# Kernel tuning notes

Measured on AMD Instinct MI355X. Metric: run time of the kernel, lower is better.

## Reference

```python
import jax, jax.numpy as jnp
import numpy as np

N = 50000      # nodes per graph
E = 600000     # edges per graph
IN_DIM = 512
HID = 128
LAYERS = 2


def setup_inputs() -> dict:
    key = jax.random.key(0)
    ks = jax.random.split(key, 24)
    s = 0.05
    inp = {
        "src_fea": jax.random.normal(ks[0], (N, IN_DIM), jnp.float32),
        "trg_fea": jax.random.normal(ks[1], (N, IN_DIM), jnp.float32),
        "src_row": jax.random.randint(ks[2], (E,), 0, N, jnp.int32),
        "src_col": jax.random.randint(ks[3], (E,), 0, N, jnp.int32),
        "trg_row": jax.random.randint(ks[4], (E,), 0, N, jnp.int32),
        "trg_col": jax.random.randint(ks[5], (E,), 0, N, jnp.int32),
        # fx: Linear(in,hid)+GELU+Linear(hid,hid)+GELU
        "fxW1": jax.random.normal(ks[6], (IN_DIM, HID), jnp.float32) * s,
        "fxb1": jnp.zeros((HID,), jnp.float32),
        "fxW2": jax.random.normal(ks[7], (HID, HID), jnp.float32) * s,
        "fxb2": jnp.zeros((HID,), jnp.float32),
        # edge_att_mlp: Linear(2h,20)+ReLU+Linear(20,10)+ReLU+Linear(10,1)+ReLU
        "eaW1": jax.random.normal(ks[8], (2 * HID, 20), jnp.float32) * s,
        "eab1": jnp.zeros((20,), jnp.float32),
        "eaW2": jax.random.normal(ks[9], (20, 10), jnp.float32) * s,
        "eab2": jnp.zeros((10,), jnp.float32),
        "eaW3": jax.random.normal(ks[10], (10, 1), jnp.float32) * s,
        "eab3": jnp.zeros((1,), jnp.float32),
        # GraphConv (PyG-style, bias=False): out = x@Wroot + agg@Wrel
        "convWroot": jax.random.normal(ks[11], (LAYERS, HID, HID), jnp.float32) * s,
        "convWrel": jax.random.normal(ks[12], (LAYERS, HID, HID), jnp.float32) * s,
    }
    return inp


def _fx(x, W1, b1, W2, b2):
    h = jax.nn.gelu(x @ W1 + b1, approximate=False)
    return jax.nn.gelu(h @ W2 + b2, approximate=False)


def _edge_att(e, eaW1, eab1, eaW2, eab2, eaW3, eab3):
    h = jax.nn.relu(e @ eaW1 + eab1)
    h = jax.nn.relu(h @ eaW2 + eab2)
    h = jax.nn.relu(h @ eaW3 + eab3)
    return jax.nn.sigmoid(h)  # [E,1]


def _graph_conv(x, row, col, ew, Wroot, Wrel):
    # message from source (row) gathered, weighted, aggregated at target (col)
    msg = ew[:, None] * x[row]                                  # [E,h]
    agg = jax.ops.segment_sum(msg, col, num_segments=N)         # [N,h]
    return x @ Wroot + agg @ Wrel


def _branch(x0, row, col, convWroot, convWrel, eaW1, eab1, eaW2, eab2, eaW3, eab3, hard):
    xs, cfds = [], []
    x = x0
    for i in range(LAYERS):
        edge_rep = jnp.concatenate([x[row], x[col]], axis=-1)    # [E,2h]
        att = _edge_att(edge_rep, eaW1, eab1, eaW2, eab2, eaW3, eab3)[:, 0]
        wc = (att + hard) * 0.5
        wo = 1.0 - wc
        x = jax.nn.soft_sign(_graph_conv(x, row, col, wc, convWroot[i], convWrel[i]))
        cfd = jax.nn.soft_sign(_graph_conv(x, row, col, wo, convWroot[i], convWrel[i]))
        xs.append(x)
        cfds.append(cfd)
    return xs, cfds


def reference(src_fea, trg_fea, src_row, src_col, trg_row, trg_col,
              fxW1, fxb1, fxW2, fxb2,
              eaW1, eab1, eaW2, eab2, eaW3, eab3,
              convWroot, convWrel):
    src1 = _fx(src_fea, fxW1, fxb1, fxW2, fxb2)
    trg1 = _fx(trg_fea, fxW1, fxb1, fxW2, fxb2)
    ea = (eaW1, eab1, eaW2, eab2, eaW3, eab3)
    xs_s, cf_s = _branch(src1, src_row, src_col, convWroot, convWrel, *ea, 0.0)
    xs_t, cf_t = _branch(trg1, trg_row, trg_col, convWroot, convWrel, *ea, 0.0)
    # stack: [src1, xs_s..., trg1, xs_t..., cf_s..., cf_t...] -> [2+2*LAYERS+2*LAYERS? no: 10, N, h]
    return jnp.stack([src1] + xs_s + [trg1] + xs_t + cf_s + cf_t, axis=0)
```

## Files before the change

### kernel.cpp

```cpp
#include <hip/hip_runtime.h>
#include <math.h>
#include <stdint.h>


typedef __attribute__((ext_vector_type(8))) short bh8;
typedef __attribute__((ext_vector_type(4))) float f4;

__device__ __forceinline__ float relu_f(float x) { return x > 0.f ? x : 0.f; }

__device__ __forceinline__ unsigned short f2bf(float f) {
    union { float f; unsigned u; } v; v.f = f;
    unsigned r = v.u + 0x7FFF + ((v.u >> 16) & 1);
    return (unsigned short)(r >> 16);
}
__device__ __forceinline__ float bf2f(unsigned short b) {
    union { unsigned u; float f; } v; v.u = ((unsigned)b) << 16;
    return v.f;
}

template<int ACT>
__device__ __forceinline__ float act_fn(float x) {
    if (ACT == 1) return 0.5f * x * (1.f + erff(x * 0.70710678118654752f));
    if (ACT == 2) return x / (1.f + fabsf(x));
    return x;
}

template<int K, int AF, int ACT, bool DUAL, bool BIAS, bool WF32, bool WB16>
__global__ __launch_bounds__(256, 2)
void mfma_gemm(const void* __restrict__ X0a, const void* __restrict__ X1a,
               const void* __restrict__ X0b, const void* __restrict__ X1b,
               const short* __restrict__ W0t, const short* __restrict__ W1t,
               const float* __restrict__ bias,
               float* __restrict__ outfA, short* __restrict__ outbA,
               float* __restrict__ outfB, short* __restrict__ outbB, int M)
{
    constexpr int BK  = 64;
    constexpr int LDA = 72;
    __shared__ short As[64 * LDA];
    __shared__ short Bs[128 * LDA];

    const int half = gridDim.x >> 1;
    int bid = blockIdx.x;
    const int g1 = bid >= half;
    bid -= g1 ? half : 0;
    const void* X0v = g1 ? X0b : X0a;
    const void* X1v = g1 ? X1b : X1a;
    float* outf = g1 ? outfB : outfA;
    short* outb = g1 ? outbB : outbA;

    const int t    = threadIdx.x;
    const int row0 = bid * 64;
    const int lane = t & 63;
    const int w    = t >> 6;
    const int wr   = w & 1;
    const int wc   = w >> 1;
    const int l15  = lane & 15;
    const int l4   = lane >> 4;

    f4 acc[2][4];
    #pragma unroll
    for (int i = 0; i < 2; ++i)
        #pragma unroll
        for (int j = 0; j < 4; ++j)
            acc[i][j] = (f4){0.f, 0.f, 0.f, 0.f};

    const int ar = t >> 3;
    const int ac = (t & 7) * 8;

    #pragma unroll 1
    for (int s = 0; s < (DUAL ? 2 : 1); ++s) {
        const float* Xf = (const float*)((DUAL && s) ? X1v : X0v);
        const short* Xb = (const short*)((DUAL && s) ? X1v : X0v);
        const short* Wt = (DUAL && s) ? W1t : W0t;
        #pragma unroll 1
        for (int k0 = 0; k0 < K; k0 += BK) {
            __syncthreads();
            #pragma unroll
            for (int p = 0; p < 2; ++p) {
                int r    = ar + p * 32;
                int grow = row0 + r;
                bh8 sv = {0, 0, 0, 0, 0, 0, 0, 0};
                if (AF == 0) {
                    if (grow < M) {
                        const float* src = Xf + (size_t)grow * K + k0 + ac;
                        float4 v0 = *(const float4*)src;
                        float4 v1 = *(const float4*)(src + 4);
                        sv[0] = (short)f2bf(v0.x); sv[1] = (short)f2bf(v0.y);
                        sv[2] = (short)f2bf(v0.z); sv[3] = (short)f2bf(v0.w);
                        sv[4] = (short)f2bf(v1.x); sv[5] = (short)f2bf(v1.y);
                        sv[6] = (short)f2bf(v1.z); sv[7] = (short)f2bf(v1.w);
                    }
                } else {
                    if (grow < M)
                        sv = *(const bh8*)(Xb + (size_t)grow * K + k0 + ac);
                }
                *(bh8*)&As[r * LDA + ac] = sv;
            }
            #pragma unroll
            for (int p = 0; p < 4; ++p) {
                int r = ar + p * 32;
                *(bh8*)&Bs[r * LDA + ac] =
                    *(const bh8*)(Wt + (size_t)r * K + k0 + ac);
            }
            __syncthreads();
            #pragma unroll
            for (int kk = 0; kk < 2; ++kk) {
                bh8 a[2], b[4];
                #pragma unroll
                for (int mi = 0; mi < 2; ++mi)
                    a[mi] = *(const bh8*)&As[(wr*32 + mi*16 + l15) * LDA + kk*32 + l4*8];
                #pragma unroll
                for (int ni = 0; ni < 4; ++ni)
                    b[ni] = *(const bh8*)&Bs[(wc*64 + ni*16 + l15) * LDA + kk*32 + l4*8];
                #pragma unroll
                for (int mi = 0; mi < 2; ++mi)
                    #pragma unroll
                    for (int ni = 0; ni < 4; ++ni)
                        acc[mi][ni] = __builtin_amdgcn_mfma_f32_16x16x32_bf16(
                            a[mi], b[ni], acc[mi][ni], 0, 0, 0);
            }
        }
    }

    #pragma unroll
    for (int mi = 0; mi < 2; ++mi) {
        #pragma unroll
        for (int ni = 0; ni < 4; ++ni) {
            int col = wc * 64 + ni * 16 + l15;
            float bv = BIAS ? bias[col] : 0.f;
            #pragma unroll
            for (int r = 0; r < 4; ++r) {
                int row = row0 + wr * 32 + mi * 16 + l4 * 4 + r;
                if (row < M) {
                    float v = act_fn<ACT>(acc[mi][ni][r] + bv);
                    if (WF32) outf[(size_t)row * 128 + col] = v;
                    if (WB16) outb[(size_t)row * 128 + col] = (short)f2bf(v);
                }
            }
        }
    }
}

__global__ __launch_bounds__(256, 2)
void pkern_both(const short* __restrict__ XbS, const short* __restrict__ XbT,
                const short* __restrict__ W56,
                short* __restrict__ PS, short* __restrict__ PT, int M)
{
    constexpr int LDA = 72;
    __shared__ short As[64 * LDA];
    __shared__ short Bs[64 * LDA];

    const int half = gridDim.x >> 1;
    int bid = blockIdx.x;
    const int g1 = bid >= half;
    bid -= g1 ? half : 0;
    const short* Xb = g1 ? XbT : XbS;
    short* P        = g1 ? PT  : PS;

    const int t    = threadIdx.x;
    const int row0 = bid * 64;
    const int lane = t & 63;
    const int w    = t >> 6;
    const int l15  = lane & 15;
    const int l4   = lane >> 4;

    f4 acc[4];
    #pragma unroll
    for (int i = 0; i < 4; ++i) acc[i] = (f4){0.f, 0.f, 0.f, 0.f};

    const int ar = t >> 3;
    const int ac = (t & 7) * 8;

    #pragma unroll 1
    for (int k0 = 0; k0 < 128; k0 += 64) {
        __syncthreads();
        #pragma unroll
        for (int p = 0; p < 2; ++p) {
            int r    = ar + p * 32;
            int grow = row0 + r;
            bh8 sv = {0, 0, 0, 0, 0, 0, 0, 0};
            if (grow < M)
                sv = *(const bh8*)(Xb + (size_t)grow * 128 + k0 + ac);
            *(bh8*)&As[r * LDA + ac] = sv;
        }
        #pragma unroll
        for (int p = 0; p < 2; ++p) {
            int r = ar + p * 32;
            *(bh8*)&Bs[r * LDA + ac] =
                *(const bh8*)(W56 + (size_t)r * 128 + k0 + ac);
        }
        __syncthreads();
        #pragma unroll
        for (int kk = 0; kk < 2; ++kk) {
            bh8 a = *(const bh8*)&As[(w * 16 + l15) * LDA + kk * 32 + l4 * 8];
            #pragma unroll
            for (int ni = 0; ni < 4; ++ni) {
                bh8 b = *(const bh8*)&Bs[(ni * 16 + l15) * LDA + kk * 32 + l4 * 8];
                acc[ni] = __builtin_amdgcn_mfma_f32_16x16x32_bf16(a, b, acc[ni], 0, 0, 0);
            }
        }
    }

    #pragma unroll
    for (int ni = 0; ni < 4; ++ni) {
        int col = ni * 16 + l15;
        #pragma unroll
        for (int r = 0; r < 4; ++r) {
            int row = row0 + w * 16 + l4 * 4 + r;
            if (row < M)
                P[(size_t)row * 64 + col] = (short)f2bf(acc[ni][r]);
        }
    }
}

__global__ void prep_all(const float* __restrict__ eaW1, const float* __restrict__ fxW1,
                         const float* __restrict__ fxW2, const float* __restrict__ convWroot,
                         const float* __restrict__ convWrel,
                         short* __restrict__ w56, short* __restrict__ fxW1t,
                         short* __restrict__ fxW2t, short* __restrict__ wrt,
                         short* __restrict__ wlt)
{
    int i = blockIdx.x * 256 + threadIdx.x;
    if (i < 64 * 128) {
        int j = i >> 7, k = i & 127;
        float v = 0.f;
        if (j < 20)                  v = eaW1[k * 20 + j];
        else if (j >= 32 && j < 52)  v = eaW1[(128 + k) * 20 + (j - 32)];
        w56[i] = (short)f2bf(v);
        return;
    }
    i -= 64 * 128;
    if (i < 512 * 128) {
        int k = i >> 7, n = i & 127;
        fxW1t[(size_t)n * 512 + k] = (short)f2bf(fxW1[i]);
        return;
    }
    i -= 512 * 128;
    if (i < 128 * 128) {
        int k = i >> 7, n = i & 127;
        fxW2t[n * 128 + k] = (short)f2bf(fxW2[i]);
        return;
    }
    i -= 128 * 128;
    if (i < 2 * 128 * 128) {
        int L = i >> 14, r = i & 16383;
        int k = r >> 7, n = r & 127;
        wrt[L * 16384 + n * 128 + k] = (short)f2bf(convWroot[i]);
        return;
    }
    i -= 2 * 128 * 128;
    if (i < 2 * 128 * 128) {
        int L = i >> 14, r = i & 16383;
        int k = r >> 7, n = r & 127;
        wlt[L * 16384 + n * 128 + k] = (short)f2bf(convWrel[i]);
    }
}

__global__ __launch_bounds__(256)
void edge_att_both(const short* __restrict__ PS, const short* __restrict__ PT,
                   const int* __restrict__ rowS, const int* __restrict__ colS,
                   const int* __restrict__ rowT, const int* __restrict__ colT,
                   const int* __restrict__ eposS, const int* __restrict__ eposT,
                   const float* __restrict__ eab1, const float* __restrict__ eaW2,
                   const float* __restrict__ eab2, const float* __restrict__ eaW3,
                   const float* __restrict__ eab3,
                   float* __restrict__ attcS, float* __restrict__ attcT, int E)
{
    __shared__ float w2[200], b2s[10], w3s[10], sb1[20], sb3;
    int t = threadIdx.x;
    if (t < 200) w2[t] = eaW2[t];
    if (t < 20)  sb1[t] = eab1[t];
    if (t < 10)  { b2s[t] = eab2[t]; w3s[t] = eaW3[t]; }
    if (t == 0)  sb3 = eab3[0];
    __syncthreads();

    int idx = blockIdx.x * 256 + t;
    if (idx >= 2 * E) return;
    const int g1 = idx >= E;
    const int e  = idx - (g1 ? E : 0);
    const short* P    = g1 ? PT : PS;
    const int*   row  = g1 ? rowT : rowS;
    const int*   col  = g1 ? colT : colS;
    const int*   epos = g1 ? eposT : eposS;
    float*       attc = g1 ? attcT : attcS;

    int r = row[e], c = col[e];
    const unsigned short* p1 = (const unsigned short*)P + (size_t)r * 64;
    const unsigned short* p2 = (const unsigned short*)P + (size_t)c * 64 + 32;

    bh8 a0 = *(const bh8*)&p1[0];
    bh8 a1 = *(const bh8*)&p1[8];
    ushort4 a2 = *(const ushort4*)&p1[16];
    bh8 b0 = *(const bh8*)&p2[0];
    bh8 b1 = *(const bh8*)&p2[8];
    ushort4 b2 = *(const ushort4*)&p2[16];

    float h1[20];
    #pragma unroll
    for (int j = 0; j < 8; ++j)
        h1[j] = relu_f(bf2f((unsigned short)a0[j]) + bf2f((unsigned short)b0[j]) + sb1[j]);
    #pragma unroll
    for (int j = 0; j < 8; ++j)
        h1[8 + j] = relu_f(bf2f((unsigned short)a1[j]) + bf2f((unsigned short)b1[j]) + sb1[8 + j]);
    h1[16] = relu_f(bf2f(a2.x) + bf2f(b2.x) + sb1[16]);
    h1[17] = relu_f(bf2f(a2.y) + bf2f(b2.y) + sb1[17]);
    h1[18] = relu_f(bf2f(a2.z) + bf2f(b2.z) + sb1[18]);
    h1[19] = relu_f(bf2f(a2.w) + bf2f(b2.w) + sb1[19]);

    float h3 = sb3;
    #pragma unroll
    for (int j2 = 0; j2 < 10; ++j2) {
        float s = b2s[j2];
        #pragma unroll
        for (int j = 0; j < 20; ++j)
            s = fmaf(h1[j], w2[j * 10 + j2], s);
        h3 = fmaf(relu_f(s), w3s[j2], h3);
    }
    h3 = relu_f(h3);
    attc[epos[e]] = 1.f / (1.f + expf(-h3));
}

__global__ void hist_both(const int* __restrict__ colS, const int* __restrict__ colT,
                          int* __restrict__ deg, int N, int E)
{
    int idx = blockIdx.x * 256 + threadIdx.x;
    if (idx >= 2 * E) return;
    const int g1 = idx >= E;
    const int e  = idx - (g1 ? E : 0);
    int c = (g1 ? colT : colS)[e];
    atomicAdd(&deg[(size_t)g1 * N + c], 1);
}

__device__ __forceinline__ int block_incl_scan(int v, int* wsum)
{
    int lane = threadIdx.x & 63;
    int w    = threadIdx.x >> 6;
    #pragma unroll
    for (int off = 1; off < 64; off <<= 1) {
        int t = __shfl_up(v, off);
        if (lane >= off) v += t;
    }
    if (lane == 63) wsum[w] = v;
    __syncthreads();
    int add = 0;
    for (int j = 0; j < w; ++j) add += wsum[j];
    return v + add;
}

__global__ __launch_bounds__(256)
void scanA_both(const int* __restrict__ deg, int* __restrict__ coffS,
                int* __restrict__ coffT, int* __restrict__ bsum, int N)
{
    __shared__ int wsum[4];
    int gy = blockIdx.y;
    const int* d = deg + (size_t)gy * N;
    int* coff    = gy ? coffT : coffS;
    int* bs      = bsum + gy * 256;
    int i = blockIdx.x * 256 + threadIdx.x;
    int orig = (i < N) ? d[i] : 0;
    int v = block_incl_scan(orig, wsum);
    if (i < N) coff[i] = v - orig;
    if (threadIdx.x == 255) bs[blockIdx.x] = v;
}

__global__ __launch_bounds__(256)
void scanB_both(const int* __restrict__ bsum, int* __restrict__ boff, int nb)
{
    __shared__ int wsum[4];
    int gy = blockIdx.y;
    const int* bs = bsum + gy * 256;
    int* bo       = boff + gy * 256;
    int tid = threadIdx.x;
    int orig = (tid < nb) ? bs[tid] : 0;
    int v = block_incl_scan(orig, wsum);
    if (tid < nb) bo[tid] = v - orig;
}

__global__ __launch_bounds__(256)
void scanC_both(int* __restrict__ coffS, int* __restrict__ coffT,
                const int* __restrict__ boff, int* __restrict__ curS,
                int* __restrict__ curT, int N, int E)
{
    int gy = blockIdx.y;
    int* coff = gy ? coffT : coffS;
    int* cur  = gy ? curT  : curS;
    const int* bo = boff + gy * 256;
    int i = blockIdx.x * 256 + threadIdx.x;
    if (i < N) {
        int v = coff[i] + bo[i >> 8];
        coff[i] = v;
        cur[i]  = v;
    }
    if (i == 0) coff[N] = E;
}

__global__ __launch_bounds__(256)
void fill_both(const int* __restrict__ rowS, const int* __restrict__ colS,
               const int* __restrict__ rowT, const int* __restrict__ colT,
               int* __restrict__ curS, int* __restrict__ curT,
               int* __restrict__ crowS, int* __restrict__ crowT,
               int* __restrict__ eposS, int* __restrict__ eposT, int E)
{
    int idx = blockIdx.x * 256 + threadIdx.x;
    if (idx >= 2 * E) return;
    const int g1 = idx >= E;
    const int e  = idx - (g1 ? E : 0);
    const int* row = g1 ? rowT : rowS;
    const int* col = g1 ? colT : colS;
    int* cur  = g1 ? curT  : curS;
    int* crow = g1 ? crowT : crowS;
    int* epos = g1 ? eposT : eposS;
    int c = col[e];
    int p = atomicAdd(&cur[c], 1);
    crow[p] = row[e];
    epos[e] = p;
}

__global__ __launch_bounds__(256)
void agg_both(const short* __restrict__ XbS, const short* __restrict__ XbT,
              const int* __restrict__ coffS, const int* __restrict__ coffT,
              const int* __restrict__ crowS, const int* __restrict__ crowT,
              const float* __restrict__ attcS, const float* __restrict__ attcT,
              short* __restrict__ aggS, short* __restrict__ aggT, int N, int mode)
{
    int ng = blockIdx.x * 4 + (threadIdx.x >> 6);
    if (ng >= 2 * N) return;
    const int g1 = ng >= N;
    const int n  = ng - (g1 ? N : 0);
    const short* Xb   = g1 ? XbT   : XbS;
    const int*   coff = g1 ? coffT : coffS;
    const int*   crow = g1 ? crowT : crowS;
    const float* atc  = g1 ? attcT : attcS;
    short*       aggb = g1 ? aggT  : aggS;

    const int lane = threadIdx.x & 63;
    const int grp  = lane >> 4;
    const int li   = lane & 15;
    const int p0 = coff[n], pe = coff[n + 1];

    float acc[8] = {0.f, 0.f, 0.f, 0.f, 0.f, 0.f, 0.f, 0.f};
    for (int p = p0 + grp; p < pe; p += 4) {
        float a = atc[p];
        float w = mode ? fmaf(-0.5f, a, 1.f) : 0.5f * a;
        int r = crow[p];
        bh8 v = *(const bh8*)&Xb[(size_t)r * 128 + li * 8];
        #pragma unroll
        for (int j = 0; j < 8; ++j)
            acc[j] = fmaf(w, bf2f((unsigned short)v[j]), acc[j]);
    }
    #pragma unroll
    for (int j = 0; j < 8; ++j) acc[j] += __shfl_xor(acc[j], 16);
    #pragma unroll
    for (int j = 0; j < 8; ++j) acc[j] += __shfl_xor(acc[j], 32);
    if (grp == 0) {
        bh8 o;
        #pragma unroll
        for (int j = 0; j < 8; ++j) o[j] = (short)f2bf(acc[j]);
        *(bh8*)&aggb[(size_t)n * 128 + li * 8] = o;
    }
}


extern "C" void kernel_launch(void* const* d_in, const int* in_sizes, int n_in,
                              void* d_out, int out_size, void* d_ws, size_t ws_size,
                              hipStream_t stream)
{
    const float* src_fea = (const float*)d_in[0];
    const float* trg_fea = (const float*)d_in[1];
    const int*   src_row = (const int*)d_in[2];
    const int*   src_col = (const int*)d_in[3];
    const int*   trg_row = (const int*)d_in[4];
    const int*   trg_col = (const int*)d_in[5];
    const float* fxW1 = (const float*)d_in[6];
    const float* fxb1 = (const float*)d_in[7];
    const float* fxW2 = (const float*)d_in[8];
    const float* fxb2 = (const float*)d_in[9];
    const float* eaW1 = (const float*)d_in[10];
    const float* eab1 = (const float*)d_in[11];
    const float* eaW2 = (const float*)d_in[12];
    const float* eab2 = (const float*)d_in[13];
    const float* eaW3 = (const float*)d_in[14];
    const float* eab3 = (const float*)d_in[15];
    const float* convWroot = (const float*)d_in[16];
    const float* convWrel  = (const float*)d_in[17];

    const int N = in_sizes[0] / 512;
    const int E = in_sizes[2];

    float* out = (float*)d_out;
    const size_t slot_sz = (size_t)N * 128;
    auto slot = [&](int i) { return out + (size_t)i * slot_sz; };

    float* fp    = (float*)d_ws;
    float* attcS = fp; fp += E;
    float* attcT = fp; fp += E;
    int* ip    = (int*)fp;
    int* deg   = ip; ip += 2 * N;
    int* bsum  = ip; ip += 512;
    int* boff  = ip; ip += 512;
    int* coffS = ip; ip += N + 2;
    int* coffT = ip; ip += N + 2;
    int* curS  = ip; ip += N;
    int* curT  = ip; ip += N;
    int* crowS = ip; ip += E;
    int* crowT = ip; ip += E;
    int* eposS = ip; ip += E;
    int* eposT = ip; ip += E;
    short* sp = (short*)((((uintptr_t)ip) + 255) & ~(uintptr_t)255);
    short* xb0   = sp; sp += slot_sz;
    short* xb1   = sp; sp += slot_sz;
    short* xsbS[2]; short* xsbT[2];
    xsbS[0] = sp; sp += slot_sz;
    xsbS[1] = sp; sp += slot_sz;
    xsbT[0] = sp; sp += slot_sz;
    xsbT[1] = sp; sp += slot_sz;
    short* aggS  = sp; sp += slot_sz;
    short* aggT  = sp; sp += slot_sz;
    short* PS    = sp; sp += (size_t)N * 64;
    short* PT    = sp; sp += (size_t)N * 64;
    short* w56   = sp; sp += 64 * 128;
    short* fxW1t = sp; sp += 128 * 512;
    short* fxW2t = sp; sp += 128 * 128;
    short* wrt   = sp; sp += 2 * 128 * 128;
    short* wlt   = sp; sp += 2 * 128 * 128;

    const int prep_total = 64*128 + 512*128 + 128*128 + 2*128*128 + 2*128*128;
    prep_all<<<(prep_total + 255) / 256, 256, 0, stream>>>(
        eaW1, fxW1, fxW2, convWroot, convWrel, w56, fxW1t, fxW2t, wrt, wlt);

    const int gb = (N + 63) / 64;
    short* hS = xsbS[0];
    short* hT = xsbT[0];
    mfma_gemm<512, 0, 1, false, true, false, true><<<2 * gb, 256, 0, stream>>>(
        src_fea, nullptr, trg_fea, nullptr, fxW1t, nullptr, fxb1,
        nullptr, hS, nullptr, hT, N);
    mfma_gemm<128, 1, 1, false, true, true, true><<<2 * gb, 256, 0, stream>>>(
        hS, nullptr, hT, nullptr, fxW2t, nullptr, fxb2,
        slot(0), xb0, slot(3), xb1, N);

    const int e2grid  = (2 * E + 255) / 256;
    const int nchunks = (N + 255) / 256;
    hipMemsetAsync(deg, 0, (size_t)2 * N * sizeof(int), stream);
    hist_both<<<e2grid, 256, 0, stream>>>(src_col, trg_col, deg, N, E);
    scanA_both<<<dim3(nchunks, 2), 256, 0, stream>>>(deg, coffS, coffT, bsum, N);
    scanB_both<<<dim3(1, 2), 256, 0, stream>>>(bsum, boff, nchunks);
    scanC_both<<<dim3(nchunks, 2), 256, 0, stream>>>(coffS, coffT, boff, curS, curT, N, E);
    fill_both<<<e2grid, 256, 0, stream>>>(src_row, src_col, trg_row, trg_col,
                                          curS, curT, crowS, crowT, eposS, eposT, E);

    const int agrid = (2 * N + 3) / 4;

    short* xbS = xb0;
    short* xbT = xb1;
    for (int L = 0; L < 2; ++L) {
        float* xs_s = slot(1 + L);
        float* xs_t = slot(4 + L);
        float* cf_s = slot(6 + L);
        float* cf_t = slot(8 + L);
        const short* WrT = wrt + (size_t)L * 16384;
        const short* WlT = wlt + (size_t)L * 16384;

        pkern_both<<<2 * gb, 256, 0, stream>>>(xbS, xbT, w56, PS, PT, N);
        edge_att_both<<<e2grid, 256, 0, stream>>>(PS, PT, src_row, src_col,
            trg_row, trg_col, eposS, eposT, eab1, eaW2, eab2, eaW3, eab3,
            attcS, attcT, E);

        agg_both<<<agrid, 256, 0, stream>>>(xbS, xbT, coffS, coffT, crowS, crowT,
                                            attcS, attcT, aggS, aggT, N, 0);
        mfma_gemm<128, 1, 2, true, false, true, true><<<2 * gb, 256, 0, stream>>>(
            xbS, aggS, xbT, aggT, WrT, WlT, nullptr,
            xs_s, xsbS[L], xs_t, xsbT[L], N);

        agg_both<<<agrid, 256, 0, stream>>>(xsbS[L], xsbT[L], coffS, coffT,
                                            crowS, crowT, attcS, attcT, aggS, aggT, N, 1);
        mfma_gemm<128, 1, 2, true, false, true, false><<<2 * gb, 256, 0, stream>>>(
            xsbS[L], aggS, xsbT[L], aggT, WrT, WlT, nullptr,
            cf_s, nullptr, cf_t, nullptr, N);

        xbS = xsbS[L];
        xbT = xsbT[L];
    }
}
```

Baseline: 689.9 us.

## Fuse neighbor aggregation into conv GEMM and fold P projection into epilogues

Removes the separate agg_both and pkern_both kernels. Each conv block now gathers its 64 rows' weighted neighbor sums directly into shared memory, then runs the Wrel and Wroot MFMA passes. The edge-attention projection P is computed in the epilogue of the preceding GEMM from the bf16 output already held in LDS. This saves the agg buffer round-trip through global memory and several kernel launches. In exchange, the gather is serialized per row inside a GEMM block (16 threads per row, 4 rows per thread group), which may lower gather parallelism and occupancy because the A tile grows to 136 shorts per row.

```diff
diff --git a/kernel.cpp b/kernel.cpp
--- a/kernel.cpp
+++ b/kernel.cpp
@@ -25,28 +25,65 @@
     return x;
 }
 
-template<int K, int AF, int ACT, bool DUAL, bool BIAS, bool WF32, bool WB16>
+__device__ __forceinline__ void emit_p_phase(short* As, short* Bs,
+                                             const short* __restrict__ W56,
+                                             short* __restrict__ P,
+                                             int row0, int M, int t)
+{
+    #pragma unroll
+    for (int p = 0; p < 4; ++p) {
+        int idx = t + 256 * p;
+        int r = idx >> 4;
+        int c = (idx & 15) * 8;
+        *(bh8*)&Bs[r * 136 + c] = *(const bh8*)(W56 + r * 128 + c);
+    }
+    __syncthreads();
+    const int lane = t & 63, w = t >> 6, l15 = lane & 15, l4 = lane >> 4;
+    f4 accP[4];
+    #pragma unroll
+    for (int ni = 0; ni < 4; ++ni) accP[ni] = (f4){0.f, 0.f, 0.f, 0.f};
+    #pragma unroll
+    for (int kk = 0; kk < 4; ++kk) {
+        bh8 a = *(const bh8*)&As[(w * 16 + l15) * 136 + kk * 32 + l4 * 8];
+        #pragma unroll
+        for (int ni = 0; ni < 4; ++ni) {
+            bh8 b = *(const bh8*)&Bs[(ni * 16 + l15) * 136 + kk * 32 + l4 * 8];
+            accP[ni] = __builtin_amdgcn_mfma_f32_16x16x32_bf16(a, b, accP[ni], 0, 0, 0);
+        }
+    }
+    #pragma unroll
+    for (int ni = 0; ni < 4; ++ni) {
+        int col = ni * 16 + l15;
+        #pragma unroll
+        for (int r = 0; r < 4; ++r) {
+            int row = row0 + w * 16 + l4 * 4 + r;
+            if (row < M) P[(size_t)row * 64 + col] = (short)f2bf(accP[ni][r]);
+        }
+    }
+}
+
+template<int K, int AF, int ACT, bool BIAS, bool WF32, bool WB16, bool EMITP>
 __global__ __launch_bounds__(256, 2)
-void mfma_gemm(const void* __restrict__ X0a, const void* __restrict__ X1a,
-               const void* __restrict__ X0b, const void* __restrict__ X1b,
-               const short* __restrict__ W0t, const short* __restrict__ W1t,
-               const float* __restrict__ bias,
+void mfma_gemm(const void* __restrict__ X0a, const void* __restrict__ X0b,
+               const short* __restrict__ W0t, const float* __restrict__ bias,
                float* __restrict__ outfA, short* __restrict__ outbA,
-               float* __restrict__ outfB, short* __restrict__ outbB, int M)
+               float* __restrict__ outfB, short* __restrict__ outbB,
+               const short* __restrict__ W56,
+               short* __restrict__ PA, short* __restrict__ PB, int M)
 {
     constexpr int BK  = 64;
-    constexpr int LDA = 72;
+    constexpr int LDA = EMITP ? 136 : 72;
     __shared__ short As[64 * LDA];
-    __shared__ short Bs[128 * LDA];
+    __shared__ short Bs[128 * 72];
 
     const int half = gridDim.x >> 1;
     int bid = blockIdx.x;
     const int g1 = bid >= half;
     bid -= g1 ? half : 0;
     const void* X0v = g1 ? X0b : X0a;
-    const void* X1v = g1 ? X1b : X1a;
     float* outf = g1 ? outfB : outfA;
     short* outb = g1 ? outbB : outbA;
+    short* P    = g1 ? PB : PA;
 
     const int t    = threadIdx.x;
     const int row0 = bid * 64;
@@ -68,60 +105,54 @@
     const int ac = (t & 7) * 8;
 
     #pragma unroll 1
-    for (int s = 0; s < (DUAL ? 2 : 1); ++s) {
-        const float* Xf = (const float*)((DUAL && s) ? X1v : X0v);
-        const short* Xb = (const short*)((DUAL && s) ? X1v : X0v);
-        const short* Wt = (DUAL && s) ? W1t : W0t;
-        #pragma unroll 1
-        for (int k0 = 0; k0 < K; k0 += BK) {
-            __syncthreads();
-            #pragma unroll
-            for (int p = 0; p < 2; ++p) {
-                int r    = ar + p * 32;
-                int grow = row0 + r;
-                bh8 sv = {0, 0, 0, 0, 0, 0, 0, 0};
-                if (AF == 0) {
-                    if (grow < M) {
-                        const float* src = Xf + (size_t)grow * K + k0 + ac;
-                        float4 v0 = *(const float4*)src;
-                        float4 v1 = *(const float4*)(src + 4);
-                        sv[0] = (short)f2bf(v0.x); sv[1] = (short)f2bf(v0.y);
-                        sv[2] = (short)f2bf(v0.z); sv[3] = (short)f2bf(v0.w);
-                        sv[4] = (short)f2bf(v1.x); sv[5] = (short)f2bf(v1.y);
-                        sv[6] = (short)f2bf(v1.z); sv[7] = (short)f2bf(v1.w);
-                    }
-                } else {
-                    if (grow < M)
-                        sv = *(const bh8*)(Xb + (size_t)grow * K + k0 + ac);
+    for (int k0 = 0; k0 < K; k0 += BK) {
+        __syncthreads();
+        #pragma unroll
+        for (int p = 0; p < 2; ++p) {
+            int r    = ar + p * 32;
+            int grow = row0 + r;
+            bh8 sv = {0, 0, 0, 0, 0, 0, 0, 0};
+            if (AF == 0) {
+                if (grow < M) {
+                    const float* src = (const float*)X0v + (size_t)grow * K + k0 + ac;
+                    float4 v0 = *(const float4*)src;
+                    float4 v1 = *(const float4*)(src + 4);
+                    sv[0] = (short)f2bf(v0.x); sv[1] = (short)f2bf(v0.y);
+                    sv[2] = (short)f2bf(v0.z); sv[3] = (short)f2bf(v0.w);
+                    sv[4] = (short)f2bf(v1.x); sv[5] = (short)f2bf(v1.y);
+                    sv[6] = (short)f2bf(v1.z); sv[7] = (short)f2bf(v1.w);
                 }
-                *(bh8*)&As[r * LDA + ac] = sv;
+            } else {
+                if (grow < M)
+                    sv = *(const bh8*)((const short*)X0v + (size_t)grow * K + k0 + ac);
             }
-            #pragma unroll
-            for (int p = 0; p < 4; ++p) {
-                int r = ar + p * 32;
-                *(bh8*)&Bs[r * LDA + ac] =
-                    *(const bh8*)(Wt + (size_t)r * K + k0 + ac);
-            }
-            __syncthreads();
-            #pragma unroll
-            for (int kk = 0; kk < 2; ++kk) {
-                bh8 a[2], b[4];
-                #pragma unroll
-                for (int mi = 0; mi < 2; ++mi)
-                    a[mi] = *(const bh8*)&As[(wr*32 + mi*16 + l15) * LDA + kk*32 + l4*8];
+            *(bh8*)&As[r * LDA + ac] = sv;
+        }
+        #pragma unroll
+        for (int p = 0; p < 4; ++p) {
+            int r = ar + p * 32;
+            *(bh8*)&Bs[r * 72 + ac] = *(const bh8*)(W0t + (size_t)r * K + k0 + ac);
+        }
+        __syncthreads();
+        #pragma unroll
+        for (int kk = 0; kk < 2; ++kk) {
+            bh8 a[2], b[4];
+            #pragma unroll
+            for (int mi = 0; mi < 2; ++mi)
+                a[mi] = *(const bh8*)&As[(wr*32 + mi*16 + l15) * LDA + kk*32 + l4*8];
+            #pragma unroll
+            for (int ni = 0; ni < 4; ++ni)
+                b[ni] = *(const bh8*)&Bs[(wc*64 + ni*16 + l15) * 72 + kk*32 + l4*8];
+            #pragma unroll
+            for (int mi = 0; mi < 2; ++mi)
                 #pragma unroll
                 for (int ni = 0; ni < 4; ++ni)
-                    b[ni] = *(const bh8*)&Bs[(wc*64 + ni*16 + l15) * LDA + kk*32 + l4*8];
-                #pragma unroll
-                for (int mi = 0; mi < 2; ++mi)
-                    #pragma unroll
-                    for (int ni = 0; ni < 4; ++ni)
-                        acc[mi][ni] = __builtin_amdgcn_mfma_f32_16x16x32_bf16(
-                            a[mi], b[ni], acc[mi][ni], 0, 0, 0);
-            }
-        }
-    }
-
+                    acc[mi][ni] = __builtin_amdgcn_mfma_f32_16x16x32_bf16(
+                        a[mi], b[ni], acc[mi][ni], 0, 0, 0);
+        }
+    }
+
+    if (EMITP) __syncthreads();
     #pragma unroll
     for (int mi = 0; mi < 2; ++mi) {
         #pragma unroll
@@ -130,46 +161,144 @@
             float bv = BIAS ? bias[col] : 0.f;
             #pragma unroll
             for (int r = 0; r < 4; ++r) {
-                int row = row0 + wr * 32 + mi * 16 + l4 * 4 + r;
+                int rloc = wr * 32 + mi * 16 + l4 * 4 + r;
+                int row  = row0 + rloc;
+                float v = act_fn<ACT>(acc[mi][ni][r] + bv);
+                unsigned short bb = f2bf(v);
                 if (row < M) {
-                    float v = act_fn<ACT>(acc[mi][ni][r] + bv);
                     if (WF32) outf[(size_t)row * 128 + col] = v;
-                    if (WB16) outb[(size_t)row * 128 + col] = (short)f2bf(v);
+                    if (WB16) outb[(size_t)row * 128 + col] = (short)bb;
                 }
+                if (EMITP) As[rloc * LDA + col] = (short)bb;
             }
         }
     }
-}
-
+    if (EMITP) emit_p_phase(As, Bs, W56, P, row0, M, t);
+}
+
+template<int MODE, bool WB16, bool EMITP>
 __global__ __launch_bounds__(256, 2)
-void pkern_both(const short* __restrict__ XbS, const short* __restrict__ XbT,
+void conv_fused(const short* __restrict__ XbA, const short* __restrict__ XbB,
+                const int* __restrict__ coffA, const int* __restrict__ coffB,
+                const int* __restrict__ crowA, const int* __restrict__ crowB,
+                const float* __restrict__ attcA, const float* __restrict__ attcB,
+                const short* __restrict__ Wroot, const short* __restrict__ Wrel,
                 const short* __restrict__ W56,
-                short* __restrict__ PS, short* __restrict__ PT, int M)
-{
-    constexpr int LDA = 72;
+                float* __restrict__ outfA, float* __restrict__ outfB,
+                short* __restrict__ outbA, short* __restrict__ outbB,
+                short* __restrict__ PA, short* __restrict__ PB, int M)
+{
+    constexpr int LDA = 136;
     __shared__ short As[64 * LDA];
-    __shared__ short Bs[64 * LDA];
+    __shared__ short Bs[128 * 72];
 
     const int half = gridDim.x >> 1;
     int bid = blockIdx.x;
     const int g1 = bid >= half;
     bid -= g1 ? half : 0;
-    const short* Xb = g1 ? XbT : XbS;
-    short* P        = g1 ? PT  : PS;
+    const short* Xb   = g1 ? XbB   : XbA;
+    const int*   coff = g1 ? coffB : coffA;
+    const int*   crow = g1 ? crowB : crowA;
+    const float* attc = g1 ? attcB : attcA;
+    float* outf = g1 ? outfB : outfA;
+    short* outb = g1 ? outbB : outbA;
+    short* P    = g1 ? PB : PA;
 
     const int t    = threadIdx.x;
     const int row0 = bid * 64;
     const int lane = t & 63;
     const int w    = t >> 6;
+    const int wr   = w & 1;
+    const int wc   = w >> 1;
     const int l15  = lane & 15;
     const int l4   = lane >> 4;
 
-    f4 acc[4];
-    #pragma unroll
-    for (int i = 0; i < 4; ++i) acc[i] = (f4){0.f, 0.f, 0.f, 0.f};
+    {
+        const int g  = t >> 4;
+        const int li = t & 15;
+        #pragma unroll 1
+        for (int q = 0; q < 4; ++q) {
+            int rloc = g * 4 + q;
+            int n = row0 + rloc;
+            float a8[8] = {0.f, 0.f, 0.f, 0.f, 0.f, 0.f, 0.f, 0.f};
+            if (n < M) {
+                int p  = coff[n];
+                int pe = coff[n + 1];
+                for (; p + 3 < pe; p += 4) {
+                    float w0 = attc[p],     w1 = attc[p + 1];
+                    float w2 = attc[p + 2], w3 = attc[p + 3];
+                    int r0 = crow[p],     r1 = crow[p + 1];
+                    int r2 = crow[p + 2], r3 = crow[p + 3];
+                    w0 = MODE ? fmaf(-0.5f, w0, 1.f) : 0.5f * w0;
+                    w1 = MODE ? fmaf(-0.5f, w1, 1.f) : 0.5f * w1;
+                    w2 = MODE ? fmaf(-0.5f, w2, 1.f) : 0.5f * w2;
+                    w3 = MODE ? fmaf(-0.5f, w3, 1.f) : 0.5f * w3;
+                    bh8 v0 = *(const bh8*)&Xb[(size_t)r0 * 128 + li * 8];
+                    bh8 v1 = *(const bh8*)&Xb[(size_t)r1 * 128 + li * 8];
+                    bh8 v2 = *(const bh8*)&Xb[(size_t)r2 * 128 + li * 8];
+                    bh8 v3 = *(const bh8*)&Xb[(size_t)r3 * 128 + li * 8];
+                    #pragma unroll
+                    for (int j = 0; j < 8; ++j) {
+                        a8[j] = fmaf(w0, bf2f((unsigned short)v0[j]), a8[j]);
+                        a8[j] = fmaf(w1, bf2f((unsigned short)v1[j]), a8[j]);
+                        a8[j] = fmaf(w2, bf2f((unsigned short)v2[j]), a8[j]);
+                        a8[j] = fmaf(w3, bf2f((unsigned short)v3[j]), a8[j]);
+                    }
+                }
+                for (; p < pe; ++p) {
+                    float w0 = attc[p];
+                    int   r0 = crow[p];
+                    w0 = MODE ? fmaf(-0.5f, w0, 1.f) : 0.5f * w0;
+                    bh8 v0 = *(const bh8*)&Xb[(size_t)r0 * 128 + li * 8];
+                    #pragma unroll
+                    for (int j = 0; j < 8; ++j)
+                        a8[j] = fmaf(w0, bf2f((unsigned short)v0[j]), a8[j]);
+                }
+            }
+            bh8 o;
+            #pragma unroll
+            for (int j = 0; j < 8; ++j) o[j] = (short)f2bf(a8[j]);
+            *(bh8*)&As[rloc * LDA + li * 8] = o;
+        }
+    }
+    __syncthreads();
+
+    f4 acc[2][4];
+    #pragma unroll
+    for (int i = 0; i < 2; ++i)
+        #pragma unroll
+        for (int j = 0; j < 4; ++j)
+            acc[i][j] = (f4){0.f, 0.f, 0.f, 0.f};
 
     const int ar = t >> 3;
     const int ac = (t & 7) * 8;
+
+    #pragma unroll 1
+    for (int k0 = 0; k0 < 128; k0 += 64) {
+        if (k0) __syncthreads();
+        #pragma unroll
+        for (int p = 0; p < 4; ++p) {
+            int r = ar + p * 32;
+            *(bh8*)&Bs[r * 72 + ac] = *(const bh8*)(Wrel + (size_t)r * 128 + k0 + ac);
+        }
+        __syncthreads();
+        #pragma unroll
+        for (int kk = 0; kk < 2; ++kk) {
+            bh8 a[2], b[4];
+            #pragma unroll
+            for (int mi = 0; mi < 2; ++mi)
+                a[mi] = *(const bh8*)&As[(wr*32 + mi*16 + l15) * LDA + k0 + kk*32 + l4*8];
+            #pragma unroll
+            for (int ni = 0; ni < 4; ++ni)
+                b[ni] = *(const bh8*)&Bs[(wc*64 + ni*16 + l15) * 72 + kk*32 + l4*8];
+            #pragma unroll
+            for (int mi = 0; mi < 2; ++mi)
+                #pragma unroll
+                for (int ni = 0; ni < 4; ++ni)
+                    acc[mi][ni] = __builtin_amdgcn_mfma_f32_16x16x32_bf16(
+                        a[mi], b[ni], acc[mi][ni], 0, 0, 0);
+        }
+    }
 
     #pragma unroll 1
     for (int k0 = 0; k0 < 128; k0 += 64) {
@@ -184,33 +313,50 @@
             *(bh8*)&As[r * LDA + ac] = sv;
         }
         #pragma unroll
-        for (int p = 0; p < 2; ++p) {
+        for (int p = 0; p < 4; ++p) {
             int r = ar + p * 32;
-            *(bh8*)&Bs[r * LDA + ac] =
-                *(const bh8*)(W56 + (size_t)r * 128 + k0 + ac);
+            *(bh8*)&Bs[r * 72 + ac] = *(const bh8*)(Wroot + (size_t)r * 128 + k0 + ac);
         }
         __syncthreads();
         #pragma unroll
         for (int kk = 0; kk < 2; ++kk) {
-            bh8 a = *(const bh8*)&As[(w * 16 + l15) * LDA + kk * 32 + l4 * 8];
-            #pragma unroll
-            for (int ni = 0; ni < 4; ++ni) {
-                bh8 b = *(const bh8*)&Bs[(ni * 16 + l15) * LDA + kk * 32 + l4 * 8];
-                acc[ni] = __builtin_amdgcn_mfma_f32_16x16x32_bf16(a, b, acc[ni], 0, 0, 0);
+            bh8 a[2], b[4];
+            #pragma unroll
+            for (int mi = 0; mi < 2; ++mi)
+                a[mi] = *(const bh8*)&As[(wr*32 + mi*16 + l15) * LDA + kk*32 + l4*8];
+            #pragma unroll
+            for (int ni = 0; ni < 4; ++ni)
+                b[ni] = *(const bh8*)&Bs[(wc*64 + ni*16 + l15) * 72 + kk*32 + l4*8];
+            #pragma unroll
+            for (int mi = 0; mi < 2; ++mi)
+                #pragma unroll
+                for (int ni = 0; ni < 4; ++ni)
+                    acc[mi][ni] = __builtin_amdgcn_mfma_f32_16x16x32_bf16(
+                        a[mi], b[ni], acc[mi][ni], 0, 0, 0);
+        }
+    }
+
+    if (EMITP) __syncthreads();
+    #pragma unroll
+    for (int mi = 0; mi < 2; ++mi) {
+        #pragma unroll
+        for (int ni = 0; ni < 4; ++ni) {
+            int col = wc * 64 + ni * 16 + l15;
+            #pragma unroll
+            for (int r = 0; r < 4; ++r) {
+                int rloc = wr * 32 + mi * 16 + l4 * 4 + r;
+                int row  = row0 + rloc;
+                float v = act_fn<2>(acc[mi][ni][r]);
+                unsigned short bb = f2bf(v);
+                if (row < M) {
+                    outf[(size_t)row * 128 + col] = v;
+                    if (WB16) outb[(size_t)row * 128 + col] = (short)bb;
+                }
+                if (EMITP) As[rloc * LDA + col] = (short)bb;
             }
         }
     }
-
-    #pragma unroll
-    for (int ni = 0; ni < 4; ++ni) {
-        int col = ni * 16 + l15;
-        #pragma unroll
-        for (int r = 0; r < 4; ++r) {
-            int row = row0 + w * 16 + l4 * 4 + r;
-            if (row < M)
-                P[(size_t)row * 64 + col] = (short)f2bf(acc[ni][r]);
-        }
-    }
+    if (EMITP) emit_p_phase(As, Bs, W56, P, row0, M, t);
 }
 
 __global__ void prep_all(const float* __restrict__ eaW1, const float* __restrict__ fxW1,
@@ -414,50 +560,6 @@
     int p = atomicAdd(&cur[c], 1);
     crow[p] = row[e];
     epos[e] = p;
-}
-
-__global__ __launch_bounds__(256)
-void agg_both(const short* __restrict__ XbS, const short* __restrict__ XbT,
-              const int* __restrict__ coffS, const int* __restrict__ coffT,
-              const int* __restrict__ crowS, const int* __restrict__ crowT,
-              const float* __restrict__ attcS, const float* __restrict__ attcT,
-              short* __restrict__ aggS, short* __restrict__ aggT, int N, int mode)
-{
-    int ng = blockIdx.x * 4 + (threadIdx.x >> 6);
-    if (ng >= 2 * N) return;
-    const int g1 = ng >= N;
-    const int n  = ng - (g1 ? N : 0);
-    const short* Xb   = g1 ? XbT   : XbS;
-    const int*   coff = g1 ? coffT : coffS;
-    const int*   crow = g1 ? crowT : crowS;
-    const float* atc  = g1 ? attcT : attcS;
-    short*       aggb = g1 ? aggT  : aggS;
-
-    const int lane = threadIdx.x & 63;
-    const int grp  = lane >> 4;
-    const int li   = lane & 15;
-    const int p0 = coff[n], pe = coff[n + 1];
-
-    float acc[8] = {0.f, 0.f, 0.f, 0.f, 0.f, 0.f, 0.f, 0.f};
-    for (int p = p0 + grp; p < pe; p += 4) {
-        float a = atc[p];
-        float w = mode ? fmaf(-0.5f, a, 1.f) : 0.5f * a;
-        int r = crow[p];
-        bh8 v = *(const bh8*)&Xb[(size_t)r * 128 + li * 8];
-        #pragma unroll
-        for (int j = 0; j < 8; ++j)
-            acc[j] = fmaf(w, bf2f((unsigned short)v[j]), acc[j]);
-    }
-    #pragma unroll
-    for (int j = 0; j < 8; ++j) acc[j] += __shfl_xor(acc[j], 16);
-    #pragma unroll
-    for (int j = 0; j < 8; ++j) acc[j] += __shfl_xor(acc[j], 32);
-    if (grp == 0) {
-        bh8 o;
-        #pragma unroll
-        for (int j = 0; j < 8; ++j) o[j] = (short)f2bf(acc[j]);
-        *(bh8*)&aggb[(size_t)n * 128 + li * 8] = o;
-    }
 }
 
 
@@ -514,8 +616,6 @@
     xsbS[1] = sp; sp += slot_sz;
     xsbT[0] = sp; sp += slot_sz;
     xsbT[1] = sp; sp += slot_sz;
-    short* aggS  = sp; sp += slot_sz;
-    short* aggT  = sp; sp += slot_sz;
     short* PS    = sp; sp += (size_t)N * 64;
     short* PT    = sp; sp += (size_t)N * 64;
     short* w56   = sp; sp += 64 * 128;
@@ -531,12 +631,12 @@
     const int gb = (N + 63) / 64;
     short* hS = xsbS[0];
     short* hT = xsbT[0];
-    mfma_gemm<512, 0, 1, false, true, false, true><<<2 * gb, 256, 0, stream>>>(
-        src_fea, nullptr, trg_fea, nullptr, fxW1t, nullptr, fxb1,
-        nullptr, hS, nullptr, hT, N);
-    mfma_gemm<128, 1, 1, false, true, true, true><<<2 * gb, 256, 0, stream>>>(
-        hS, nullptr, hT, nullptr, fxW2t, nullptr, fxb2,
-        slot(0), xb0, slot(3), xb1, N);
+    mfma_gemm<512, 0, 1, true, false, true, false><<<2 * gb, 256, 0, stream>>>(
+        src_fea, trg_fea, fxW1t, fxb1,
+        nullptr, hS, nullptr, hT, nullptr, nullptr, nullptr, N);
+    mfma_gemm<128, 1, 1, true, true, true, true><<<2 * gb, 256, 0, stream>>>(
+        hS, hT, fxW2t, fxb2,
+        slot(0), xb0, slot(3), xb1, w56, PS, PT, N);
 
     const int e2grid  = (2 * E + 255) / 256;
     const int nchunks = (N + 255) / 256;
@@ -548,8 +648,6 @@
     fill_both<<<e2grid, 256, 0, stream>>>(src_row, src_col, trg_row, trg_col,
                                           curS, curT, crowS, crowT, eposS, eposT, E);
 
-    const int agrid = (2 * N + 3) / 4;
-
     short* xbS = xb0;
     short* xbT = xb1;
     for (int L = 0; L < 2; ++L) {
@@ -560,22 +658,22 @@
         const short* WrT = wrt + (size_t)L * 16384;
         const short* WlT = wlt + (size_t)L * 16384;
 
-        pkern_both<<<2 * gb, 256, 0, stream>>>(xbS, xbT, w56, PS, PT, N);
         edge_att_both<<<e2grid, 256, 0, stream>>>(PS, PT, src_row, src_col,
             trg_row, trg_col, eposS, eposT, eab1, eaW2, eab2, eaW3, eab3,
             attcS, attcT, E);
 
-        agg_both<<<agrid, 256, 0, stream>>>(xbS, xbT, coffS, coffT, crowS, crowT,
-                                            attcS, attcT, aggS, aggT, N, 0);
-        mfma_gemm<128, 1, 2, true, false, true, true><<<2 * gb, 256, 0, stream>>>(
-            xbS, aggS, xbT, aggT, WrT, WlT, nullptr,
-            xs_s, xsbS[L], xs_t, xsbT[L], N);
-
-        agg_both<<<agrid, 256, 0, stream>>>(xsbS[L], xsbT[L], coffS, coffT,
-                                            crowS, crowT, attcS, attcT, aggS, aggT, N, 1);
-        mfma_gemm<128, 1, 2, true, false, true, false><<<2 * gb, 256, 0, stream>>>(
-            xsbS[L], aggS, xsbT[L], aggT, WrT, WlT, nullptr,
-            cf_s, nullptr, cf_t, nullptr, N);
+        if (L == 0)
+            conv_fused<0, true, true><<<2 * gb, 256, 0, stream>>>(
+                xbS, xbT, coffS, coffT, crowS, crowT, attcS, attcT,
+                WrT, WlT, w56, xs_s, xs_t, xsbS[L], xsbT[L], PS, PT, N);
+        else
+            conv_fused<0, true, false><<<2 * gb, 256, 0, stream>>>(
+                xbS, xbT, coffS, coffT, crowS, crowT, attcS, attcT,
+                WrT, WlT, nullptr, xs_s, xs_t, xsbS[L], xsbT[L], nullptr, nullptr, N);
+
+        conv_fused<1, false, false><<<2 * gb, 256, 0, stream>>>(
+            xsbS[L], xsbT[L], coffS, coffT, crowS, crowT, attcS, attcT,
+            WrT, WlT, nullptr, cf_s, cf_t, nullptr, nullptr, nullptr, nullptr, N);
 
         xbS = xsbS[L];
         xbT = xsbT[L];
```

Measured after the change: 652.7 us. 5.4% less time.
